# Performance work log

Measured on AMD Instinct MI355X. Metric: run time of the kernel, lower is better.

Reference implementation:

```python
import jax, jax.numpy as jnp
import numpy as np

# ---- configuration (matches init_kwargs / input_specs) ----
N = 48        # velocity grid points per axis (unum = vnum = wnum)
B = 8         # spatial cells (batch)
QUAD = 8      # radial Gauss-Legendre quadrature points
OMEGA = 0.81  # VHS exponent used in the radial kernel weight r**omega
M_ANG = 5     # sphere-quadrature resolution -> M*(M-1) angle pairs
VMAX = 5.0    # velocity domain [-VMAX, VMAX]^3


def _besselj1(x):
    # Numerical Recipes rational approximation of J1(x), numpy, setup-time only.
    x = np.asarray(x, dtype=np.float64)
    ax = np.abs(x)
    y = x * x
    p1 = x * (72362614232.0 + y * (-7895059235.0 + y * (242396853.1
         + y * (-2972611.439 + y * (15704.48260 + y * (-30.16036606))))))
    q1 = 144725228442.0 + y * (2300535178.0 + y * (18583304.74
         + y * (99447.43394 + y * (376.9991397 + y))))
    small = p1 / q1
    axs = np.where(ax > 0, ax, 1.0)
    z = 8.0 / axs
    y2 = z * z
    p2 = 1.0 + y2 * (0.183105e-2 + y2 * (-0.3516396496e-4
         + y2 * (0.2457520174e-5 + y2 * (-0.240337019e-6))))
    q2 = 0.04687499995 + y2 * (-0.2002690873e-3 + y2 * (0.8449199096e-5
         + y2 * (-0.88228987e-6 + y2 * 0.105787412e-6)))
    xx = axs - 2.356194491  # ax - 3*pi/4
    big = np.sqrt(0.636619772 / axs) * (np.cos(xx) * p2 - z * np.sin(xx) * q2) * np.sign(x)
    return np.where(ax < 8.0, small, big)


def _init_kernel_mode_vector(n, quad_num, omega, m, vmax):
    # Fast spectral method precompute (Mouhot-Pareschi), mirrors init_kernel_mode_vector.
    pi = np.pi
    du = 2.0 * vmax / (n - 1)
    fre = np.arange(-(n // 2), n // 2).astype(np.float64) * (2.0 * pi / (n * du))
    supp = np.sqrt(2.0) * 2.0 * vmax / (3.0 + np.sqrt(2.0))
    xg, wg = np.polynomial.legendre.leggauss(quad_num)  # on [-1,1]
    r = 0.5 * supp * (xg + 1.0)   # radial abscissa on [0, supp]
    gw = 0.5 * supp * wg          # radial weights
    ta = pi / m * np.arange(1, m)      # (m-1,) polar angles
    tb = pi / m * np.arange(1, m + 1)  # (m,)  azimuthal angles
    st = np.sin(ta)[:, None, None, None, None]
    ct = np.cos(ta)[:, None, None, None, None]
    cb = np.cos(tb)[None, :, None, None, None]
    sb = np.sin(tb)[None, :, None, None, None]
    fx = fre[:, None, None]
    fy = fre[None, :, None]
    fz = fre[None, None, :]
    # s[a,b,i,j,k] = <freq, sigma(theta_a, theta2_b)>
    s = st * cb * fx + st * sb * fy + (ct * np.ones_like(sb)) * fz
    phi = np.zeros_like(s)
    for q in range(quad_num):  # small fixed quadrature loop (setup only)
        phi += 2.0 * gw[q] * (r[q] ** omega) * np.cos(s * r[q])
    phi *= st
    s2 = (fx ** 2 + fy ** 2 + fz ** 2) - s ** 2
    pos = s2 > 1e-12
    sr = np.sqrt(np.where(pos, s2, 1.0))
    psi = np.where(pos, 2.0 * pi * supp * _besselj1(supp * sr) / sr, pi * supp ** 2)
    phipsi = (phi * psi).sum(axis=(0, 1))
    t = (m - 1) * m
    return (phi.reshape(t, n, n, n).astype(np.float32),
            psi.reshape(t, n, n, n).astype(np.float32),
            phipsi.astype(np.float32))


def setup_inputs() -> dict:
    key = jax.random.key(0)
    k1, _ = jax.random.split(key)
    phi, psi, phipsi = _init_kernel_mode_vector(N, QUAD, OMEGA, M_ANG, VMAX)
    f = jax.random.uniform(k1, (B, N * N * N), dtype=jnp.float32)
    return {
        "f": f,
        "kn_bzm": jnp.ones((), dtype=jnp.float32),
        "phi": jnp.asarray(phi),
        "psi": jnp.asarray(psi),
        "phipsi": jnp.asarray(phipsi),
        "M": M_ANG,
    }


def reference(f, kn_bzm, phi, psi, phipsi, M):
    # do_collision: reshape flat velocity dim to 3D grid, run collision_fft.
    n = phi.shape[-1]
    axes = (-3, -2, -1)
    f3 = f.reshape(f.shape[:-1] + (n, n, n))
    nvel = n * n * n
    # normalized, shifted spectrum of f
    f_spec = jnp.fft.fftshift(
        jnp.fft.fftn(f3.astype(jnp.complex64), axes=axes) / nvel, axes=axes)
    # gain term: sum over M*(M-1) angle pairs of fft(f_spec*phi_t) * fft(f_spec*psi_t)
    fs = f_spec[..., None, :, :, :]                       # [B, 1, n, n, n]
    fg = (jnp.fft.fftn(fs * phi, axes=axes) *
          jnp.fft.fftn(fs * psi, axes=axes)).sum(axis=-4)  # [B, n, n, n]
    # loss term
    fl = (jnp.fft.fftn(f_spec * phipsi, axes=axes) *
          jnp.fft.fftn(f_spec, axes=axes))
    scale = (4.0 * jnp.pi ** 2) / kn_bzm / (M * M)
    Q = scale * (fg - fl).real
    return Q.reshape(f.shape).astype(f.dtype)
```

## Files before the change

kernel.cpp:

```cpp
#include <hip/hip_runtime.h>
#include <math.h>

#define NN 48
#define NP 49
#define N2 2304
#define N3 110592
#define NB 8
#define NT 20
#define NH 25
#define NSL 7

typedef float2 cplx;

#define CMAC(AR, AI, D, Wv)                                        \
    AR = fmaf((D).x, (Wv).x, AR); AR = fmaf(-(D).y, (Wv).y, AR);   \
    AI = fmaf((D).x, (Wv).y, AI); AI = fmaf((D).y, (Wv).x, AI);

#define CMAC4(AC, D, Wv)                                             \
    (AC).x = fmaf((D).x, (Wv).x, (AC).x); (AC).x = fmaf(-(D).y, (Wv).y, (AC).x); \
    (AC).y = fmaf((D).x, (Wv).y, (AC).y); (AC).y = fmaf((D).y, (Wv).x, (AC).y); \
    (AC).z = fmaf((D).z, (Wv).x, (AC).z); (AC).z = fmaf(-(D).w, (Wv).y, (AC).z); \
    (AC).w = fmaf((D).z, (Wv).y, (AC).w); (AC).w = fmaf((D).w, (Wv).x, (AC).w);

__device__ __forceinline__ void twinit(cplx* W, int t) {
    if (t < NN) {
        float ang = -6.28318530717958647692f * (float)t / (float)NN;
        float s, c;
        sincosf(ang, &s, &c);
        W[t] = make_float2(c, s);
    }
}

__device__ __forceinline__ void radix3_combine(
    float s0r, float s0i, float s1r, float s1i, float s2r, float s2i,
    cplx w1, cplx w2, cplx& X0, cplx& X1, cplx& X2)
{
    float y1r = s1r*w1.x - s1i*w1.y, y1i = s1r*w1.y + s1i*w1.x;
    float y2r = s2r*w2.x - s2i*w2.y, y2i = s2r*w2.y + s2i*w2.x;
    float ar = y1r + y2r, ai = y1i + y2i;
    float br = y1r - y2r, bi = y1i - y2i;
    X0 = make_float2(s0r + ar, s0i + ai);
    float mr = s0r - 0.5f*ar, mi = s0i - 0.5f*ai;
    const float h = 0.86602540378443864676f;
    X1 = make_float2(mr + h*bi, mi - h*br);
    X2 = make_float2(mr - h*bi, mi + h*br);
}

__device__ __forceinline__ void radix3_combine4(
    float4 s0, float4 s1, float4 s2, cplx w1, cplx w2,
    float4& X0, float4& X1, float4& X2)
{
    cplx a0, a1, a2, b0, b1, b2;
    radix3_combine(s0.x, s0.y, s1.x, s1.y, s2.x, s2.y, w1, w2, a0, a1, a2);
    radix3_combine(s0.z, s0.w, s1.z, s1.w, s2.z, s2.w, w1, w2, b0, b1, b2);
    X0 = make_float4(a0.x, a0.y, b0.x, b0.y);
    X1 = make_float4(a1.x, a1.y, b1.x, b1.y);
    X2 = make_float4(a2.x, a2.y, b2.x, b2.y);
}

__device__ __forceinline__ void dft_rows(cplx (*S)[NP], const cplx* W, int t, int shift) {
    const int rg = t >> 4;
    const int j  = t & 15;
    float ar[3][3], ai[3][3];
#pragma unroll
    for (int q = 0; q < 3; ++q)
#pragma unroll
        for (int r = 0; r < 3; ++r) { ar[q][r] = 0.f; ai[q][r] = 0.f; }
    const int step = 3 * j;
    int tw = 0;
#pragma unroll 4
    for (int n1 = 0; n1 < 16; ++n1) {
        cplx w = W[tw];
#pragma unroll
        for (int q = 0; q < 3; ++q) {
            const cplx* row = S[3*rg + q];
            cplx d0 = row[3*n1+0], d1 = row[3*n1+1], d2 = row[3*n1+2];
            CMAC(ar[q][0], ai[q][0], d0, w);
            CMAC(ar[q][1], ai[q][1], d1, w);
            CMAC(ar[q][2], ai[q][2], d2, w);
        }
        tw += step; if (tw >= NN) tw -= NN;
    }
    cplx w1 = W[j], w2 = W[2*j];
    __syncthreads();
    int k0 = j, k1 = j + 16, k2 = j + 32;
    if (shift) { k0 = (k0+24)%NN; k1 = (k1+24)%NN; k2 = (k2+24)%NN; }
#pragma unroll
    for (int q = 0; q < 3; ++q) {
        cplx X0, X1, X2;
        radix3_combine(ar[q][0],ai[q][0],ar[q][1],ai[q][1],ar[q][2],ai[q][2],w1,w2,X0,X1,X2);
        S[3*rg+q][k0] = X0; S[3*rg+q][k1] = X1; S[3*rg+q][k2] = X2;
    }
    __syncthreads();
}

__device__ __forceinline__ void dft_cols(cplx (*S)[NP], const cplx* W, int t, int shift) {
    const int zg = t & 15;
    const int j  = t >> 4;
    float ar[3][3], ai[3][3];
#pragma unroll
    for (int zi = 0; zi < 3; ++zi)
#pragma unroll
        for (int r = 0; r < 3; ++r) { ar[zi][r] = 0.f; ai[zi][r] = 0.f; }
    const int step = 3 * j;
    int tw = 0;
#pragma unroll 4
    for (int n1 = 0; n1 < 16; ++n1) {
        cplx w = W[tw];
#pragma unroll
        for (int r = 0; r < 3; ++r) {
            const cplx* row = S[3*n1 + r];
            cplx d0 = row[3*zg+0], d1 = row[3*zg+1], d2 = row[3*zg+2];
            CMAC(ar[0][r], ai[0][r], d0, w);
            CMAC(ar[1][r], ai[1][r], d1, w);
            CMAC(ar[2][r], ai[2][r], d2, w);
        }
        tw += step; if (tw >= NN) tw -= NN;
    }
    cplx w1 = W[j], w2 = W[2*j];
    __syncthreads();
    int k0 = j, k1 = j + 16, k2 = j + 32;
    if (shift) { k0 = (k0+24)%NN; k1 = (k1+24)%NN; k2 = (k2+24)%NN; }
#pragma unroll
    for (int zi = 0; zi < 3; ++zi) {
        cplx X0, X1, X2;
        radix3_combine(ar[zi][0],ai[zi][0],ar[zi][1],ai[zi][1],ar[zi][2],ai[zi][2],w1,w2,X0,X1,X2);
        S[k0][3*zg+zi] = X0; S[k1][3*zg+zi] = X1; S[k2][3*zg+zi] = X2;
    }
    __syncthreads();
}

__device__ __forceinline__ void dft_rows4(float4 (*S)[NP], const cplx* W, int t) {
    const int rg = t >> 4;
    const int j  = t & 15;
    float4 acc[3][3];
#pragma unroll
    for (int q = 0; q < 3; ++q)
#pragma unroll
        for (int r = 0; r < 3; ++r) acc[q][r] = make_float4(0.f,0.f,0.f,0.f);
    const int step = 3 * j;
    int tw = 0;
    const float4* r0 = S[3*rg + 0];
    const float4* r1 = S[3*rg + 1];
    const float4* r2 = S[3*rg + 2];
#pragma unroll 4
    for (int n1 = 0; n1 < 16; ++n1) {
        cplx w = W[tw];
        float4 d00 = r0[3*n1+0], d01 = r0[3*n1+1], d02 = r0[3*n1+2];
        float4 d10 = r1[3*n1+0], d11 = r1[3*n1+1], d12 = r1[3*n1+2];
        float4 d20 = r2[3*n1+0], d21 = r2[3*n1+1], d22 = r2[3*n1+2];
        CMAC4(acc[0][0], d00, w); CMAC4(acc[0][1], d01, w); CMAC4(acc[0][2], d02, w);
        CMAC4(acc[1][0], d10, w); CMAC4(acc[1][1], d11, w); CMAC4(acc[1][2], d12, w);
        CMAC4(acc[2][0], d20, w); CMAC4(acc[2][1], d21, w); CMAC4(acc[2][2], d22, w);
        tw += step; if (tw >= NN) tw -= NN;
    }
    cplx w1 = W[j], w2 = W[2*j];
    __syncthreads();
#pragma unroll
    for (int q = 0; q < 3; ++q) {
        float4 X0, X1, X2;
        radix3_combine4(acc[q][0], acc[q][1], acc[q][2], w1, w2, X0, X1, X2);
        S[3*rg+q][j] = X0; S[3*rg+q][j+16] = X1; S[3*rg+q][j+32] = X2;
    }
    __syncthreads();
}

__device__ __forceinline__ void dft_cols4(float4 (*S)[NP], const cplx* W, int t) {
    const int zg = t & 15;
    const int j  = t >> 4;
    float4 acc[3][3];
#pragma unroll
    for (int zi = 0; zi < 3; ++zi)
#pragma unroll
        for (int r = 0; r < 3; ++r) acc[zi][r] = make_float4(0.f,0.f,0.f,0.f);
    const int step = 3 * j;
    int tw = 0;
#pragma unroll 4
    for (int n1 = 0; n1 < 16; ++n1) {
        cplx w = W[tw];
#pragma unroll
        for (int r = 0; r < 3; ++r) {
            const float4* row = S[3*n1 + r];
            float4 d0 = row[3*zg+0], d1 = row[3*zg+1], d2 = row[3*zg+2];
            CMAC4(acc[0][r], d0, w);
            CMAC4(acc[1][r], d1, w);
            CMAC4(acc[2][r], d2, w);
        }
        tw += step; if (tw >= NN) tw -= NN;
    }
    cplx w1 = W[j], w2 = W[2*j];
    __syncthreads();
#pragma unroll
    for (int zi = 0; zi < 3; ++zi) {
        float4 X0, X1, X2;
        radix3_combine4(acc[zi][0], acc[zi][1], acc[zi][2], w1, w2, X0, X1, X2);
        S[j][3*zg+zi] = X0; S[j+16][3*zg+zi] = X1; S[j+32][3*zg+zi] = X2;
    }
    __syncthreads();
}

__global__ __launch_bounds__(256)
void kA_f(const float* __restrict__ f, cplx* __restrict__ out) {
    __shared__ cplx S[NN][NP];
    __shared__ cplx W[NN];
    const int x = blockIdx.x, b = blockIdx.y, t = threadIdx.x;
    const float* src = f + (size_t)b * N3 + (size_t)x * N2;
    for (int i = t; i < N2; i += 256) S[i / NN][i % NN] = make_float2(src[i], 0.f);
    twinit(W, t);
    __syncthreads();
    dft_rows(S, W, t, 1);
    dft_cols(S, W, t, 1);
    cplx* dst = out + (size_t)b * N3 + (size_t)x * N2;
    for (int i = t; i < N2; i += 256) dst[i] = S[i / NN][i % NN];
}

__global__ __launch_bounds__(256)
void kB_f(cplx* __restrict__ vol) {
    __shared__ cplx S[NN][NP];
    __shared__ cplx W[NN];
    const int y = blockIdx.x, b = blockIdx.y, t = threadIdx.x;
    cplx* base = vol + (size_t)b * N3 + (size_t)y * NN;
    for (int i = t; i < N2; i += 256) { int xr = i / NN, z = i % NN; S[xr][z] = base[(size_t)xr * N2 + z]; }
    twinit(W, t);
    __syncthreads();
    dft_cols(S, W, t, 1);
    const float inv = 1.f / (float)N3;
    for (int i = t; i < N2; i += 256) {
        int xr = i / NN, z = i % NN;
        cplx v = S[xr][z];
        base[(size_t)xr * N2 + z] = make_float2(v.x * inv, v.y * inv);
    }
}

__global__ __launch_bounds__(256)
void kAB(const cplx* __restrict__ spec,
         const float* __restrict__ phi, const float* __restrict__ psi,
         const float* __restrict__ phipsi,
         float4* __restrict__ vab, int t0) {
    __shared__ float4 S[NN][NP];
    __shared__ cplx W[NN];
    const int ix = blockIdx.x, b = blockIdx.y, lt = blockIdx.z, t = threadIdx.x;
    const int ti = t0 + lt;
    const cplx* src = spec + (size_t)b * N3 + (size_t)ix * N2;
    const float* mp;
    const float* mq;
    if (ti < NT) { mp = phi + (size_t)ti * N3 + (size_t)ix * N2; mq = psi + (size_t)ti * N3 + (size_t)ix * N2; }
    else         { mp = phipsi + (size_t)ix * N2;               mq = (const float*)nullptr; }
    for (int i = t; i < N2; i += 256) {
        cplx v = src[i];
        float p = mp[i];
        float q = mq ? mq[i] : 1.f;
        S[i / NN][i % NN] = make_float4(v.x * p, v.y * p, v.x * q, v.y * q);
    }
    twinit(W, t);
    __syncthreads();
    dft_rows4(S, W, t);
    dft_cols4(S, W, t);
    float4* out = vab + ((size_t)(lt * NB + b) * NH + ix) * N2;
    for (int i = t; i < N2; i += 256) out[i] = S[i / NN][i % NN];
}

__global__ __launch_bounds__(256)
void kB_all(const float4* __restrict__ vab,
            float* __restrict__ out, const float* __restrict__ kn,
            const int* __restrict__ Mv, int t0, int cn) {
    __shared__ float4 SAB[NH][NN];
    __shared__ cplx W[NN];
    const int y = blockIdx.x, b = blockIdx.y, s = blockIdx.z, t = threadIdx.x;
    twinit(W, t);
    const int zg = t & 15, jg = t >> 4;
    const int i4 = 1024 + t;
    float4* SF = (float4*)SAB;
    float qr[3][3];
#pragma unroll
    for (int m = 0; m < 3; ++m)
#pragma unroll
        for (int zi = 0; zi < 3; ++zi) qr[m][zi] = 0.f;

    float4 R0, R1, R2, R3, R4;
    {
        const float4* base = vab + (size_t)(s * NB + b) * NH * N2 + (size_t)y * NN;
        R0 = base[(size_t)((t          ) / NN) * N2 + ((t          ) % NN)];
        R1 = base[(size_t)((t +  256   ) / NN) * N2 + ((t +  256   ) % NN)];
        R2 = base[(size_t)((t +  512   ) / NN) * N2 + ((t +  512   ) % NN)];
        R3 = base[(size_t)((t +  768   ) / NN) * N2 + ((t +  768   ) % NN)];
        if (i4 < NH * NN) R4 = base[(size_t)(i4 / NN) * N2 + (i4 % NN)];
    }

    for (int lt = s; lt < cn; lt += NSL) {
        const int ti = t0 + lt;
        SF[t]        = R0;
        SF[t +  256] = R1;
        SF[t +  512] = R2;
        SF[t +  768] = R3;
        if (i4 < NH * NN) SF[i4] = R4;
        __syncthreads();
        if (lt + NSL < cn) {
            const float4* base = vab + (size_t)((lt + NSL) * NB + b) * NH * N2 + (size_t)y * NN;
            R0 = base[(size_t)((t          ) / NN) * N2 + ((t          ) % NN)];
            R1 = base[(size_t)((t +  256   ) / NN) * N2 + ((t +  256   ) % NN)];
            R2 = base[(size_t)((t +  512   ) / NN) * N2 + ((t +  512   ) % NN)];
            R3 = base[(size_t)((t +  768   ) / NN) * N2 + ((t +  768   ) % NN)];
            if (i4 < NH * NN) R4 = base[(size_t)(i4 / NN) * N2 + (i4 % NN)];
        }
        float sa[3][3], sb[3][3];
#pragma unroll
        for (int m = 0; m < 3; ++m)
#pragma unroll
            for (int zi = 0; zi < 3; ++zi) { sa[m][zi] = 0.f; sb[m][zi] = 0.f; }
        int m0 = jg, m1 = jg + 16, m2 = jg + 32;
        const int s0 = jg, s1 = jg + 16, s2 = jg + 32;
        for (int n = 1; n <= 23; ++n) {
            cplx w0 = W[m0], w1 = W[m1], w2 = W[m2];
#pragma unroll
            for (int zi = 0; zi < 3; ++zi) {
                float4 d = SAB[n][3 * zg + zi];
                sa[0][zi] = fmaf(d.x, w0.x, sa[0][zi]); sa[0][zi] = fmaf(-d.y, w0.y, sa[0][zi]);
                sa[1][zi] = fmaf(d.x, w1.x, sa[1][zi]); sa[1][zi] = fmaf(-d.y, w1.y, sa[1][zi]);
                sa[2][zi] = fmaf(d.x, w2.x, sa[2][zi]); sa[2][zi] = fmaf(-d.y, w2.y, sa[2][zi]);
                sb[0][zi] = fmaf(d.z, w0.x, sb[0][zi]); sb[0][zi] = fmaf(-d.w, w0.y, sb[0][zi]);
                sb[1][zi] = fmaf(d.z, w1.x, sb[1][zi]); sb[1][zi] = fmaf(-d.w, w1.y, sb[1][zi]);
                sb[2][zi] = fmaf(d.z, w2.x, sb[2][zi]); sb[2][zi] = fmaf(-d.w, w2.y, sb[2][zi]);
            }
            m0 += s0; if (m0 >= NN) m0 -= NN;
            m1 += s1; if (m1 >= NN) m1 -= NN;
            m2 += s2; if (m2 >= NN) m2 -= NN;
        }
        const float sgn = (jg & 1) ? -1.f : 1.f;
        const float wgt = (ti == NT) ? -1.f : 1.f;
#pragma unroll
        for (int zi = 0; zi < 3; ++zi) {
            float4 e0  = SAB[0][3 * zg + zi];
            float4 e24 = SAB[24][3 * zg + zi];
            float basea = e0.x + sgn * e24.x;
            float baseb = e0.z + sgn * e24.z;
#pragma unroll
            for (int m = 0; m < 3; ++m) {
                float Ah = basea + 2.f * sa[m][zi];
                float Bh = baseb + 2.f * sb[m][zi];
                qr[m][zi] += wgt * Ah * Bh;
            }
        }
        __syncthreads();
    }
    float mf = (float)(Mv[0] * Mv[0]);
    float scale = 4.f * 3.14159265358979323846f * 3.14159265358979323846f / (kn[0] * mf);
#pragma unroll
    for (int m = 0; m < 3; ++m) {
        int j = jg + 16 * m;
#pragma unroll
        for (int zi = 0; zi < 3; ++zi) {
            int z = 3 * zg + zi;
            size_t idx = (size_t)b * N3 + (size_t)j * N2 + (size_t)y * NN + z;
            atomicAdd(&out[idx], scale * qr[m][zi]);
        }
    }
}

extern "C" void kernel_launch(void* const* d_in, const int* in_sizes, int n_in,
                              void* d_out, int out_size, void* d_ws, size_t ws_size,
                              hipStream_t stream) {
    const float* f      = (const float*)d_in[0];
    const float* kn     = (const float*)d_in[1];
    const float* phi    = (const float*)d_in[2];
    const float* psi    = (const float*)d_in[3];
    const float* phipsi = (const float*)d_in[4];
    const int*   Mv     = (const int*)d_in[5];
    float* out = (float*)d_out;

    char* w = (char*)d_ws;
    const size_t fspecB = (size_t)NB * N3 * sizeof(cplx);
    const size_t perTB  = (size_t)NB * NH * N2 * sizeof(float4);
    cplx* fspec = (cplx*)w;
    char* pool  = w + fspecB;

    const int NTOT = NT + 1;
    size_t avail = (ws_size > fspecB) ? (ws_size - fspecB) : 0;
    int chunk = (int)(avail / perTB);
    if (chunk < 1)    chunk = 1;
    if (chunk > NTOT) chunk = NTOT;
    float4* vab = (float4*)pool;

    hipMemsetAsync(out, 0, (size_t)NB * N3 * sizeof(float), stream);

    kA_f<<<dim3(NN, NB), 256, 0, stream>>>(f, fspec);
    kB_f<<<dim3(NN, NB), 256, 0, stream>>>(fspec);

    for (int t0 = 0; t0 < NTOT; t0 += chunk) {
        int cn = (t0 + chunk <= NTOT) ? chunk : (NTOT - t0);
        kAB<<<dim3(NH, NB, cn), 256, 0, stream>>>(fspec, phi, psi, phipsi, vab, t0);
        kB_all<<<dim3(NN, NB, NSL), 256, 0, stream>>>(vab, out, kn, Mv, t0, cn);
    }
}
```

Baseline: 269.2 us.

## Loop kAB blocks over several angle slices with register prefetch of masks

kAB now launches at most seven z-blocks. Each block loops over several angle indices instead of handling a single one. The f-spectrum row is loaded into registers once and reused across those slices, and the next slice's phi/psi masks are loaded while the current slice's DFTs run. This is meant to cut redundant spectrum loads and hide global load latency, at the cost of fewer blocks in flight and more registers per thread. kB_all's z dimension is also clamped to the chunk count.

```diff
diff --git a/kernel.cpp b/kernel.cpp
--- a/kernel.cpp
+++ b/kernel.cpp
@@ -9,6 +9,7 @@
 #define NT 20
 #define NH 25
 #define NSL 7
+#define TSL 7
 
 typedef float2 cplx;
 
@@ -236,28 +237,65 @@
 void kAB(const cplx* __restrict__ spec,
          const float* __restrict__ phi, const float* __restrict__ psi,
          const float* __restrict__ phipsi,
-         float4* __restrict__ vab, int t0) {
+         float4* __restrict__ vab, int t0, int cn) {
     __shared__ float4 S[NN][NP];
     __shared__ cplx W[NN];
-    const int ix = blockIdx.x, b = blockIdx.y, lt = blockIdx.z, t = threadIdx.x;
-    const int ti = t0 + lt;
-    const cplx* src = spec + (size_t)b * N3 + (size_t)ix * N2;
-    const float* mp;
-    const float* mq;
-    if (ti < NT) { mp = phi + (size_t)ti * N3 + (size_t)ix * N2; mq = psi + (size_t)ti * N3 + (size_t)ix * N2; }
-    else         { mp = phipsi + (size_t)ix * N2;               mq = (const float*)nullptr; }
-    for (int i = t; i < N2; i += 256) {
-        cplx v = src[i];
-        float p = mp[i];
-        float q = mq ? mq[i] : 1.f;
-        S[i / NN][i % NN] = make_float4(v.x * p, v.y * p, v.x * q, v.y * q);
-    }
+    const int ix = blockIdx.x, b = blockIdx.y, s = blockIdx.z, t = threadIdx.x;
     twinit(W, t);
-    __syncthreads();
-    dft_rows4(S, W, t);
-    dft_cols4(S, W, t);
-    float4* out = vab + ((size_t)(lt * NB + b) * NH + ix) * N2;
-    for (int i = t; i < N2; i += 256) out[i] = S[i / NN][i % NN];
+
+    cplx sp[9];
+    {
+        const cplx* src = spec + (size_t)b * N3 + (size_t)ix * N2;
+#pragma unroll
+        for (int k = 0; k < 9; ++k) sp[k] = src[t + 256 * k];
+    }
+
+    float p[9], q[9];
+    {
+        const int ti = t0 + s;
+        if (ti < NT) {
+            const float* mp = phi + (size_t)ti * N3 + (size_t)ix * N2;
+            const float* mq = psi + (size_t)ti * N3 + (size_t)ix * N2;
+#pragma unroll
+            for (int k = 0; k < 9; ++k) { p[k] = mp[t + 256 * k]; q[k] = mq[t + 256 * k]; }
+        } else {
+            const float* mp = phipsi + (size_t)ix * N2;
+#pragma unroll
+            for (int k = 0; k < 9; ++k) { p[k] = mp[t + 256 * k]; q[k] = 1.f; }
+        }
+    }
+
+    for (int lt = s; lt < cn; lt += TSL) {
+#pragma unroll
+        for (int k = 0; k < 9; ++k) {
+            int i = t + 256 * k;
+            S[i / NN][i % NN] = make_float4(sp[k].x * p[k], sp[k].y * p[k],
+                                            sp[k].x * q[k], sp[k].y * q[k]);
+        }
+        __syncthreads();
+        const int ltn = lt + TSL;
+        if (ltn < cn) {
+            const int ti = t0 + ltn;
+            if (ti < NT) {
+                const float* mp = phi + (size_t)ti * N3 + (size_t)ix * N2;
+                const float* mq = psi + (size_t)ti * N3 + (size_t)ix * N2;
+#pragma unroll
+                for (int k = 0; k < 9; ++k) { p[k] = mp[t + 256 * k]; q[k] = mq[t + 256 * k]; }
+            } else {
+                const float* mp = phipsi + (size_t)ix * N2;
+#pragma unroll
+                for (int k = 0; k < 9; ++k) { p[k] = mp[t + 256 * k]; q[k] = 1.f; }
+            }
+        }
+        dft_rows4(S, W, t);
+        dft_cols4(S, W, t);
+        float4* out = vab + ((size_t)(lt * NB + b) * NH + ix) * N2;
+#pragma unroll
+        for (int k = 0; k < 9; ++k) {
+            int i = t + 256 * k;
+            out[i] = S[i / NN][i % NN];
+        }
+    }
 }
 
 __global__ __launch_bounds__(256)
@@ -388,7 +426,9 @@
 
     for (int t0 = 0; t0 < NTOT; t0 += chunk) {
         int cn = (t0 + chunk <= NTOT) ? chunk : (NTOT - t0);
-        kAB<<<dim3(NH, NB, cn), 256, 0, stream>>>(fspec, phi, psi, phipsi, vab, t0);
-        kB_all<<<dim3(NN, NB, NSL), 256, 0, stream>>>(vab, out, kn, Mv, t0, cn);
-    }
-}
+        int zk = (cn < TSL) ? cn : TSL;
+        kAB<<<dim3(NH, NB, zk), 256, 0, stream>>>(fspec, phi, psi, phipsi, vab, t0, cn);
+        int zb = (cn < NSL) ? cn : NSL;
+        kB_all<<<dim3(NN, NB, zb), 256, 0, stream>>>(vab, out, kn, Mv, t0, cn);
+    }
+}
```

Result: slower. 280.1 us (+4.1%).
